# Kernel tuning notes

Hardware: AMD Instinct MI355X
Metric: run time of the kernel (lower is better)

Reference implementation:

```python
import jax, jax.numpy as jnp
import numpy as np

DK = 128
B, S = 16, 2048

def setup_inputs() -> dict:
    key = jax.random.key(0)
    kq, kk, kv = jax.random.split(key, 3)
    q = jax.random.normal(kq, (B, S, DK), dtype=jnp.float32)
    k = jax.random.normal(kk, (B, S, DK), dtype=jnp.float32)
    v = jax.random.normal(kv, (B, S, DK), dtype=jnp.float32)
    return {"q": q, "k": k, "v": v}

def reference(q, k, v):
    # scores: [B, S, S]
    scale = 1.0 / jnp.sqrt(jnp.float32(DK))
    scores = jnp.einsum("bqd,bkd->bqk", q, k) * scale
    probs = jax.nn.softmax(scores, axis=-1)
    # dropout is identity in eval mode (training=None)
    return jnp.einsum("bqk,bkd->bqd", probs, v)
```

## Files before the change

kernel.cpp:

```cpp
#include <hip/hip_runtime.h>
#include <hip/hip_bf16.h>

#define BATCH 16
#define SEQ   2048
#define DK    128
#define NT    16
#define SC2   0.12751744f
#define THRL2 11.541560f

typedef __attribute__((ext_vector_type(8)))  short short8v;
typedef __attribute__((ext_vector_type(4)))  float float4v;
typedef __attribute__((ext_vector_type(16))) float float16v;

typedef const __attribute__((address_space(1))) unsigned int* gas_t;
typedef __attribute__((address_space(3))) unsigned int* las_t;

__device__ inline void gl_lds16(const void* g, void* l) {
    __builtin_amdgcn_global_load_lds((gas_t)g, (las_t)l, 16, 0, 0);
}

__device__ inline short f2bf(float f) {
    __hip_bfloat16 h = __float2bfloat16(f);
    unsigned short u;
    __builtin_memcpy(&u, &h, sizeof(u));
    return (short)u;
}

__device__ inline unsigned cvt_pk_bf16(float a, float b) {
    unsigned r;
    asm("v_cvt_pk_bf16_f32 %0, %1, %2" : "=v"(r) : "v"(a), "v"(b));
    return r;
}

__global__ __launch_bounds__(256)
void conv_k_kernel(const float* __restrict__ k, short* __restrict__ kb)
{
    size_t i = ((size_t)blockIdx.x * 256 + threadIdx.x) * 8;
    float4 a = *reinterpret_cast<const float4*>(k + i);
    float4 b = *reinterpret_cast<const float4*>(k + i + 4);
    short8v t;
    t[0] = f2bf(a.x * SC2); t[1] = f2bf(a.y * SC2); t[2] = f2bf(a.z * SC2); t[3] = f2bf(a.w * SC2);
    t[4] = f2bf(b.x * SC2); t[5] = f2bf(b.y * SC2); t[6] = f2bf(b.z * SC2); t[7] = f2bf(b.w * SC2);
    *reinterpret_cast<short8v*>(kb + i) = t;
}

__global__ __launch_bounds__(256)
void transpose_v_kernel(const float* __restrict__ v, short* __restrict__ vt)
{
    __shared__ float tile[32][33];
    const int tx = threadIdx.x & 31;
    const int ty = threadIdx.x >> 5;
    const int b  = blockIdx.z;
    const int s0 = blockIdx.x * 32;
    const int d0 = blockIdx.y * 32;

    const float* vb = v + ((size_t)b * SEQ + s0) * DK + d0;
#pragma unroll
    for (int i = 0; i < 4; ++i) {
        int r = ty + 8 * i;
        tile[r][tx] = vb[(size_t)r * DK + tx];
    }
    __syncthreads();

    const int s   = s0 + tx;
    const int kvl = s & 15;
    const int pos = (((kvl >> 2) & 1) << 3) | (((kvl >> 3) & 1) << 2) | (kvl & 3);
    const size_t col = (size_t)(s & ~15) | pos;

    short* vtb = vt + ((size_t)b * DK + d0) * SEQ;
#pragma unroll
    for (int i = 0; i < 4; ++i) {
        int r = ty + 8 * i;
        vtb[(size_t)r * SEQ + col] = f2bf(tile[tx][r]);
    }
}

__global__ __launch_bounds__(512, 2)
void attn_fwd_v6(const float* __restrict__ q,
                 const short* __restrict__ kb,
                 const short* __restrict__ vt,
                 float* __restrict__ out)
{
    __shared__ __align__(16) char lds[131072];

    const int tid  = threadIdx.x;
    const int lane = tid & 63;
    const int wave = tid >> 6;
    const int qt   = wave & 3;
    const int h    = wave >> 2;
    const int b    = blockIdx.y;
    const int q0   = blockIdx.x * 128 + qt * 32;

    const int l31 = lane & 31;
    const int hi  = lane >> 5;

    const float* qrow = q + ((size_t)b * SEQ + q0 + l31) * DK + hi * 8;
    short8v qf[8];
#pragma unroll
    for (int s = 0; s < 8; ++s) {
        float4 x = *reinterpret_cast<const float4*>(qrow + s * 16);
        float4 y = *reinterpret_cast<const float4*>(qrow + s * 16 + 4);
        union { unsigned u[4]; short8v v; } pk;
        pk.u[0] = cvt_pk_bf16(x.x, x.y);
        pk.u[1] = cvt_pk_bf16(x.z, x.w);
        pk.u[2] = cvt_pk_bf16(y.x, y.y);
        pk.u[3] = cvt_pk_bf16(y.z, y.w);
        qf[s] = pk.v;
    }

    const char* kB = (const char*)(kb + (size_t)b * SEQ * DK);
    const char* vB = (const char*)(vt + (size_t)b * DK * SEQ);
    const int hkv = h * 1024;

    const char* src[8];
    int dstoff[8];
    long sstep;
    if (qt < 2) {
#pragma unroll
        for (int i = 0; i < 8; ++i) {
            const int kr = qt * 32 + i * 4 + (lane >> 4);
            src[i] = kB + (size_t)(hkv + kr) * 256 + (((lane & 15) ^ (kr & 15)) << 4);
            dstoff[i] = h * 32768 + qt * 8192 + i * 1024;
        }
        sstep = 64 * 256;
    } else {
#pragma unroll
        for (int i = 0; i < 8; ++i) {
            const int R  = (qt - 2) * 32 + i * 4 + (lane >> 4);
            const int wx = (lane & 15) ^ (R & 15);
            const int d  = 2 * R + (wx >> 3);
            src[i] = vB + (size_t)d * (SEQ * 2) + (size_t)hkv * 2 + ((wx & 7) << 4);
            dstoff[i] = h * 32768 + 16384 + (qt - 2) * 8192 + i * 1024;
        }
        sstep = 64 * 2;
    }

    float m_run = -1e30f;
    float l_run = 0.0f;
    float16v o[4];
#pragma unroll
    for (int dblk = 0; dblk < 4; ++dblk)
#pragma unroll
        for (int i = 0; i < 16; ++i) o[dblk][i] = 0.f;

    auto STAGE = [&](int bufsel, int t) {
        char* base = lds + bufsel * 65536;
#pragma unroll
        for (int i = 0; i < 8; ++i)
            gl_lds16(src[i] + (size_t)t * sstep, base + dstoff[i]);
    };

    STAGE(0, 0);
    __syncthreads();

    int buf = 0;
    for (int t = 0; t < NT; ++t) {
        if (t + 1 < NT) STAGE(buf ^ 1, t + 1);

        const char* Kl = lds + buf * 65536 + h * 32768;
        const char* Vl = Kl + 16384;
        const char* ka = Kl + l31 * 256;

        float16v sa[2];
#pragma unroll
        for (int i = 0; i < 16; ++i) { sa[0][i] = 0.f; sa[1][i] = 0.f; }
        __builtin_amdgcn_s_setprio(1);
#pragma unroll
        for (int s = 0; s < 8; ++s) {
            const int un = ((2 * s + hi) ^ (l31 & 15)) << 4;
            short8v kf0 = *reinterpret_cast<const short8v*>(ka + un);
            short8v kf1 = *reinterpret_cast<const short8v*>(ka + 8192 + un);
            sa[0] = __builtin_amdgcn_mfma_f32_32x32x16_bf16(kf0, qf[s], sa[0], 0, 0, 0);
            sa[1] = __builtin_amdgcn_mfma_f32_32x32x16_bf16(kf1, qf[s], sa[1], 0, 0, 0);
        }
        __builtin_amdgcn_s_setprio(0);

        float mx = sa[0][0];
#pragma unroll
        for (int i = 1; i < 16; ++i) mx = fmaxf(mx, sa[0][i]);
#pragma unroll
        for (int i = 0; i < 16; ++i) mx = fmaxf(mx, sa[1][i]);
        mx = fmaxf(mx, __shfl_xor(mx, 32));

        if (!__all(mx <= m_run + THRL2)) {
            const float mnew  = fmaxf(m_run, mx);
            const float alpha = exp2f(m_run - mnew);
            l_run *= alpha;
            m_run = mnew;
            float aq[16];
#pragma unroll
            for (int reg = 0; reg < 16; ++reg)
                aq[reg] = __shfl(alpha, (reg & 3) + 8 * (reg >> 2) + 4 * hi);
#pragma unroll
            for (int dblk = 0; dblk < 4; ++dblk)
#pragma unroll
                for (int reg = 0; reg < 16; ++reg) o[dblk][reg] *= aq[reg];
        }

        float ts = 0.f;
#pragma unroll
        for (int sub = 0; sub < 2; ++sub)
#pragma unroll
            for (int i = 0; i < 16; ++i) {
                const float e = exp2f(sa[sub][i] - m_run);
                sa[sub][i] = e;
                ts += e;
            }
        ts += __shfl_xor(ts, 32);
        l_run += ts;

        short8v pf[4];
#pragma unroll
        for (int g = 0; g < 4; ++g) {
            const int sub = g >> 1, r0 = (g & 1) * 8;
            union { unsigned u[4]; short8v v; } pk;
            pk.u[0] = cvt_pk_bf16(sa[sub][r0 + 0], sa[sub][r0 + 1]);
            pk.u[1] = cvt_pk_bf16(sa[sub][r0 + 2], sa[sub][r0 + 3]);
            pk.u[2] = cvt_pk_bf16(sa[sub][r0 + 4], sa[sub][r0 + 5]);
            pk.u[3] = cvt_pk_bf16(sa[sub][r0 + 6], sa[sub][r0 + 7]);
            pf[g] = pk.v;
        }

        __builtin_amdgcn_s_setprio(1);
#pragma unroll
        for (int dblk = 0; dblk < 4; ++dblk) {
            const int R  = dblk * 16 + (l31 >> 1);
            const char* vr = Vl + R * 256;
            const int dh = (l31 & 1) << 3;
#pragma unroll
            for (int g = 0; g < 4; ++g) {
                const int w = ((dh | (2 * g + hi)) ^ (R & 15)) << 4;
                short8v vf = *reinterpret_cast<const short8v*>(vr + w);
                o[dblk] = __builtin_amdgcn_mfma_f32_32x32x16_bf16(pf[g], vf, o[dblk], 0, 0, 0);
            }
        }
        __builtin_amdgcn_s_setprio(0);

        __syncthreads();
        buf ^= 1;
    }

    float* smO = (float*)lds;
    float* smM = (float*)(lds + 65536);
    float* smL = (float*)(lds + 66048);

    if (h == 1) {
        if (hi == 0) { smM[qt * 32 + l31] = m_run; smL[qt * 32 + l31] = l_run; }
#pragma unroll
        for (int dblk = 0; dblk < 4; ++dblk)
#pragma unroll
            for (int reg = 0; reg < 16; ++reg) {
                const int qp = (reg & 3) + 8 * (reg >> 2) + 4 * hi;
                smO[(qt * 32 + qp) * 128 + dblk * 32 + l31] = o[dblk][reg];
            }
    }
    __syncthreads();
    if (h == 0) {
        const float m1 = smM[qt * 32 + l31];
        const float l1 = smL[qt * 32 + l31];
        const float mf = fmaxf(m_run, m1);
        const float a0 = exp2f(m_run - mf);
        const float a1 = exp2f(m1 - mf);
        const float li = 1.0f / (l_run * a0 + l1 * a1);
        const float w0 = a0 * li;
        const float w1 = a1 * li;

        float w0q[16], w1q[16];
#pragma unroll
        for (int reg = 0; reg < 16; ++reg) {
            const int qp = (reg & 3) + 8 * (reg >> 2) + 4 * hi;
            w0q[reg] = __shfl(w0, qp);
            w1q[reg] = __shfl(w1, qp);
        }

        float* ob = out + ((size_t)b * SEQ + q0) * DK;
#pragma unroll
        for (int dblk = 0; dblk < 4; ++dblk)
#pragma unroll
            for (int reg = 0; reg < 16; ++reg) {
                const int qp = (reg & 3) + 8 * (reg >> 2) + 4 * hi;
                ob[(size_t)qp * DK + dblk * 32 + l31] =
                    o[dblk][reg] * w0q[reg]
                    + smO[(qt * 32 + qp) * 128 + dblk * 32 + l31] * w1q[reg];
            }
    }
}

__global__ __launch_bounds__(256)
void attn_fwd_slow(const float* __restrict__ q,
                   const float* __restrict__ k,
                   const float* __restrict__ v,
                   float* __restrict__ out)
{
    const int lane = threadIdx.x & 63;
    const int wave = threadIdx.x >> 6;
    const int b    = blockIdx.y;
    const int q0   = blockIdx.x * 64 + wave * 16;
    const int row = lane & 15;
    const int grp = lane >> 4;

    const float* qb = q + ((size_t)b * SEQ + q0) * DK;
    const float* kbp = k + (size_t)b * SEQ * DK;
    const float* vbp = v + (size_t)b * SEQ * DK;

    short8v qf[4];
#pragma unroll
    for (int c = 0; c < 4; ++c) {
        const float* p = qb + row * DK + c * 32 + grp * 8;
        float4 x = *reinterpret_cast<const float4*>(p);
        float4 y = *reinterpret_cast<const float4*>(p + 4);
        short8v t;
        t[0] = f2bf(x.x); t[1] = f2bf(x.y); t[2] = f2bf(x.z); t[3] = f2bf(x.w);
        t[4] = f2bf(y.x); t[5] = f2bf(y.y); t[6] = f2bf(y.z); t[7] = f2bf(y.w);
        qf[c] = t;
    }

    float m_run = -1e30f, l_run = 0.0f;
    float4v o[8];
#pragma unroll
    for (int i = 0; i < 8; ++i) { o[i][0]=0.f; o[i][1]=0.f; o[i][2]=0.f; o[i][3]=0.f; }
    const float scale = 0.08838834764831845f;

    for (int kv0 = 0; kv0 < SEQ; kv0 += 16) {
        short8v kf[4];
        const float* kp0 = kbp + (size_t)(kv0 + row) * DK + grp * 8;
#pragma unroll
        for (int c = 0; c < 4; ++c) {
            const float* p = kp0 + c * 32;
            float4 x = *reinterpret_cast<const float4*>(p);
            float4 y = *reinterpret_cast<const float4*>(p + 4);
            short8v t;
            t[0] = f2bf(x.x); t[1] = f2bf(x.y); t[2] = f2bf(x.z); t[3] = f2bf(x.w);
            t[4] = f2bf(y.x); t[5] = f2bf(y.y); t[6] = f2bf(y.z); t[7] = f2bf(y.w);
            kf[c] = t;
        }
        short8v vf[8];
#pragma unroll
        for (int dblk = 0; dblk < 8; ++dblk) {
            const float* p = vbp + (size_t)(kv0 + 4 * grp) * DK + dblk * 16 + row;
            short b0 = f2bf(p[0]);
            short b1 = f2bf(p[DK]);
            short b2 = f2bf(p[2 * DK]);
            short b3 = f2bf(p[3 * DK]);
            short8v t;
            t[0]=b0; t[1]=b1; t[2]=b2; t[3]=b3; t[4]=b0; t[5]=b1; t[6]=b2; t[7]=b3;
            vf[dblk] = t;
        }
        float4v s; s[0]=0.f; s[1]=0.f; s[2]=0.f; s[3]=0.f;
#pragma unroll
        for (int c = 0; c < 4; ++c)
            s = __builtin_amdgcn_mfma_f32_16x16x32_bf16(kf[c], qf[c], s, 0, 0, 0);

        float sv[4]; float tmax = -1e30f;
#pragma unroll
        for (int r = 0; r < 4; ++r) { sv[r] = s[r] * scale; tmax = fmaxf(tmax, sv[r]); }
        tmax = fmaxf(tmax, __shfl_xor(tmax, 16));
        tmax = fmaxf(tmax, __shfl_xor(tmax, 32));
        const float mnew = fmaxf(m_run, tmax);
        float pr[4]; float tsum = 0.f;
#pragma unroll
        for (int r = 0; r < 4; ++r) { pr[r] = __expf(sv[r] - mnew); tsum += pr[r]; }
        tsum += __shfl_xor(tsum, 16);
        tsum += __shfl_xor(tsum, 32);
        const float alpha = __expf(m_run - mnew);
        l_run = l_run * alpha + tsum;
        m_run = mnew;
        float aq[4];
#pragma unroll
        for (int r = 0; r < 4; ++r) aq[r] = __shfl(alpha, grp * 4 + r);
#pragma unroll
        for (int dblk = 0; dblk < 8; ++dblk)
#pragma unroll
            for (int r = 0; r < 4; ++r) o[dblk][r] *= aq[r];

        short8v pfv;
        pfv[0]=f2bf(pr[0]); pfv[1]=f2bf(pr[1]); pfv[2]=f2bf(pr[2]); pfv[3]=f2bf(pr[3]);
        pfv[4]=0; pfv[5]=0; pfv[6]=0; pfv[7]=0;
#pragma unroll
        for (int dblk = 0; dblk < 8; ++dblk)
            o[dblk] = __builtin_amdgcn_mfma_f32_16x16x32_bf16(pfv, vf[dblk], o[dblk], 0, 0, 0);
    }

    const float linv = 1.0f / l_run;
    float li[4];
#pragma unroll
    for (int r = 0; r < 4; ++r) li[r] = __shfl(linv, grp * 4 + r);
    float* ob = out + ((size_t)b * SEQ + q0) * DK;
#pragma unroll
    for (int dblk = 0; dblk < 8; ++dblk)
#pragma unroll
        for (int r = 0; r < 4; ++r)
            ob[(size_t)(grp * 4 + r) * DK + dblk * 16 + row] = o[dblk][r] * li[r];
}

extern "C" void kernel_launch(void* const* d_in, const int* in_sizes, int n_in,
                              void* d_out, int out_size, void* d_ws, size_t ws_size,
                              hipStream_t stream) {
    const float* q = (const float*)d_in[0];
    const float* k = (const float*)d_in[1];
    const float* v = (const float*)d_in[2];
    float* out = (float*)d_out;

    const size_t kb_bytes = (size_t)BATCH * SEQ * DK * sizeof(short);
    const size_t need = 2 * kb_bytes;

    if (ws_size >= need) {
        short* kb = (short*)d_ws;
        short* vt = (short*)((char*)d_ws + kb_bytes);
        hipLaunchKernelGGL(conv_k_kernel, dim3(2048), dim3(256), 0, stream, k, kb);
        hipLaunchKernelGGL(transpose_v_kernel, dim3(SEQ / 32, DK / 32, BATCH), dim3(256), 0, stream, v, vt);
        hipLaunchKernelGGL(attn_fwd_v6, dim3(SEQ / 128, BATCH), dim3(512), 0, stream, q, kb, vt, out);
    } else {
        hipLaunchKernelGGL(attn_fwd_slow, dim3(SEQ / 64, BATCH), dim3(256), 0, stream, q, k, v, out);
    }
}
```

Measured before the change: 64.62 us.

## Halve KV tile to 32 keys, shrink LDS, raise occupancy and swizzle block mapping

Each KV tile now holds 32 keys per half instead of 64, so the flash loop runs twice as many iterations with half the LDS per buffer. LDS drops to about 65KB and the launch bound asks for 4 blocks per CU instead of 2, which should help hide latency. Staging is rebalanced so waves 0-3 load K and waves 4-7 load V, with a new swizzle pattern for the V tile. The grid is flattened to 1D with an XCD-aware remap that keeps same-batch blocks together for L2 reuse. The cost is more barriers and more softmax rescale checks per key, and less MFMA work per synchronization.

```diff
diff --git a/kernel.cpp b/kernel.cpp
--- a/kernel.cpp
+++ b/kernel.cpp
@@ -4,7 +4,7 @@
 #define BATCH 16
 #define SEQ   2048
 #define DK    128
-#define NT    16
+#define NT    32
 #define SC2   0.12751744f
 #define THRL2 11.541560f
 
@@ -75,21 +75,23 @@
     }
 }
 
-__global__ __launch_bounds__(512, 2)
-void attn_fwd_v6(const float* __restrict__ q,
+__global__ __launch_bounds__(512, 4)
+void attn_fwd_v7(const float* __restrict__ q,
                  const short* __restrict__ kb,
                  const short* __restrict__ vt,
                  float* __restrict__ out)
 {
-    __shared__ __align__(16) char lds[131072];
+    __shared__ __align__(16) char lds[66560];
 
     const int tid  = threadIdx.x;
     const int lane = tid & 63;
     const int wave = tid >> 6;
     const int qt   = wave & 3;
     const int h    = wave >> 2;
-    const int b    = blockIdx.y;
-    const int q0   = blockIdx.x * 128 + qt * 32;
+    const int bid  = blockIdx.x;
+    const int work = (bid & 7) * 32 + (bid >> 3);
+    const int b    = work >> 4;
+    const int q0   = (work & 15) * 128 + qt * 32;
 
     const int l31 = lane & 31;
     const int hi  = lane >> 5;
@@ -110,29 +112,33 @@
 
     const char* kB = (const char*)(kb + (size_t)b * SEQ * DK);
     const char* vB = (const char*)(vt + (size_t)b * DK * SEQ);
-    const int hkv = h * 1024;
-
-    const char* src[8];
-    int dstoff[8];
+
+    const char* src[4];
+    int dstoff[4];
     long sstep;
-    if (qt < 2) {
-#pragma unroll
-        for (int i = 0; i < 8; ++i) {
-            const int kr = qt * 32 + i * 4 + (lane >> 4);
-            src[i] = kB + (size_t)(hkv + kr) * 256 + (((lane & 15) ^ (kr & 15)) << 4);
-            dstoff[i] = h * 32768 + qt * 8192 + i * 1024;
-        }
-        sstep = 64 * 256;
+    if (wave < 4) {
+#pragma unroll
+        for (int i = 0; i < 4; ++i) {
+            const int c  = wave * 4 + i;
+            const int hh = c >> 3, cc = c & 7;
+            const int kr = cc * 4 + (lane >> 4);
+            src[i] = kB + (size_t)(hh * 1024 + kr) * 256
+                        + (((lane & 15) ^ (kr & 15)) << 4);
+            dstoff[i] = hh * 16384 + cc * 1024;
+        }
+        sstep = 32 * 256;
     } else {
 #pragma unroll
-        for (int i = 0; i < 8; ++i) {
-            const int R  = (qt - 2) * 32 + i * 4 + (lane >> 4);
-            const int wx = (lane & 15) ^ (R & 15);
-            const int d  = 2 * R + (wx >> 3);
-            src[i] = vB + (size_t)d * (SEQ * 2) + (size_t)hkv * 2 + ((wx & 7) << 4);
-            dstoff[i] = h * 32768 + 16384 + (qt - 2) * 8192 + i * 1024;
-        }
-        sstep = 64 * 2;
+        for (int i = 0; i < 4; ++i) {
+            const int c    = (wave - 4) * 4 + i;
+            const int hh   = c >> 3, cc = c & 7;
+            const int R    = cc * 8 + (lane >> 3);
+            const int unit = (lane & 7) ^ (R & 7);
+            const int d    = 2 * R + (unit >> 2);
+            src[i] = vB + (size_t)d * (SEQ * 2) + hh * 2048 + (unit & 3) * 16;
+            dstoff[i] = hh * 16384 + 8192 + cc * 1024;
+        }
+        sstep = 32 * 2;
     }
 
     float m_run = -1e30f;
@@ -144,9 +150,9 @@
         for (int i = 0; i < 16; ++i) o[dblk][i] = 0.f;
 
     auto STAGE = [&](int bufsel, int t) {
-        char* base = lds + bufsel * 65536;
-#pragma unroll
-        for (int i = 0; i < 8; ++i)
+        char* base = lds + bufsel * 32768;
+#pragma unroll
+        for (int i = 0; i < 4; ++i)
             gl_lds16(src[i] + (size_t)t * sstep, base + dstoff[i]);
     };
 
@@ -157,29 +163,25 @@
     for (int t = 0; t < NT; ++t) {
         if (t + 1 < NT) STAGE(buf ^ 1, t + 1);
 
-        const char* Kl = lds + buf * 65536 + h * 32768;
-        const char* Vl = Kl + 16384;
+        const char* Kl = lds + buf * 32768 + h * 16384;
+        const char* Vl = Kl + 8192;
         const char* ka = Kl + l31 * 256;
 
-        float16v sa[2];
-#pragma unroll
-        for (int i = 0; i < 16; ++i) { sa[0][i] = 0.f; sa[1][i] = 0.f; }
+        float16v sa;
+#pragma unroll
+        for (int i = 0; i < 16; ++i) sa[i] = 0.f;
         __builtin_amdgcn_s_setprio(1);
 #pragma unroll
         for (int s = 0; s < 8; ++s) {
             const int un = ((2 * s + hi) ^ (l31 & 15)) << 4;
-            short8v kf0 = *reinterpret_cast<const short8v*>(ka + un);
-            short8v kf1 = *reinterpret_cast<const short8v*>(ka + 8192 + un);
-            sa[0] = __builtin_amdgcn_mfma_f32_32x32x16_bf16(kf0, qf[s], sa[0], 0, 0, 0);
-            sa[1] = __builtin_amdgcn_mfma_f32_32x32x16_bf16(kf1, qf[s], sa[1], 0, 0, 0);
+            short8v kf = *reinterpret_cast<const short8v*>(ka + un);
+            sa = __builtin_amdgcn_mfma_f32_32x32x16_bf16(kf, qf[s], sa, 0, 0, 0);
         }
         __builtin_amdgcn_s_setprio(0);
 
-        float mx = sa[0][0];
-#pragma unroll
-        for (int i = 1; i < 16; ++i) mx = fmaxf(mx, sa[0][i]);
-#pragma unroll
-        for (int i = 0; i < 16; ++i) mx = fmaxf(mx, sa[1][i]);
+        float mx = sa[0];
+#pragma unroll
+        for (int i = 1; i < 16; ++i) mx = fmaxf(mx, sa[i]);
         mx = fmaxf(mx, __shfl_xor(mx, 32));
 
         if (!__all(mx <= m_run + THRL2)) {
@@ -199,25 +201,23 @@
 
         float ts = 0.f;
 #pragma unroll
-        for (int sub = 0; sub < 2; ++sub)
-#pragma unroll
-            for (int i = 0; i < 16; ++i) {
-                const float e = exp2f(sa[sub][i] - m_run);
-                sa[sub][i] = e;
-                ts += e;
-            }
+        for (int i = 0; i < 16; ++i) {
+            const float e = exp2f(sa[i] - m_run);
+            sa[i] = e;
+            ts += e;
+        }
         ts += __shfl_xor(ts, 32);
         l_run += ts;
 
-        short8v pf[4];
-#pragma unroll
-        for (int g = 0; g < 4; ++g) {
-            const int sub = g >> 1, r0 = (g & 1) * 8;
+        short8v pf[2];
+#pragma unroll
+        for (int g = 0; g < 2; ++g) {
+            const int r0 = g * 8;
             union { unsigned u[4]; short8v v; } pk;
-            pk.u[0] = cvt_pk_bf16(sa[sub][r0 + 0], sa[sub][r0 + 1]);
-            pk.u[1] = cvt_pk_bf16(sa[sub][r0 + 2], sa[sub][r0 + 3]);
-            pk.u[2] = cvt_pk_bf16(sa[sub][r0 + 4], sa[sub][r0 + 5]);
-            pk.u[3] = cvt_pk_bf16(sa[sub][r0 + 6], sa[sub][r0 + 7]);
+            pk.u[0] = cvt_pk_bf16(sa[r0 + 0], sa[r0 + 1]);
+            pk.u[1] = cvt_pk_bf16(sa[r0 + 2], sa[r0 + 3]);
+            pk.u[2] = cvt_pk_bf16(sa[r0 + 4], sa[r0 + 5]);
+            pk.u[3] = cvt_pk_bf16(sa[r0 + 6], sa[r0 + 7]);
             pf[g] = pk.v;
         }
 
@@ -225,11 +225,11 @@
 #pragma unroll
         for (int dblk = 0; dblk < 4; ++dblk) {
             const int R  = dblk * 16 + (l31 >> 1);
-            const char* vr = Vl + R * 256;
-            const int dh = (l31 & 1) << 3;
-#pragma unroll
-            for (int g = 0; g < 4; ++g) {
-                const int w = ((dh | (2 * g + hi)) ^ (R & 15)) << 4;
+            const char* vr = Vl + R * 128;
+            const int dh4 = (l31 & 1) << 2;
+#pragma unroll
+            for (int g = 0; g < 2; ++g) {
+                const int w = ((dh4 | (2 * g + hi)) ^ (R & 7)) << 4;
                 short8v vf = *reinterpret_cast<const short8v*>(vr + w);
                 o[dblk] = __builtin_amdgcn_mfma_f32_32x32x16_bf16(pf[g], vf, o[dblk], 0, 0, 0);
             }
@@ -409,7 +409,7 @@
         short* vt = (short*)((char*)d_ws + kb_bytes);
         hipLaunchKernelGGL(conv_k_kernel, dim3(2048), dim3(256), 0, stream, k, kb);
         hipLaunchKernelGGL(transpose_v_kernel, dim3(SEQ / 32, DK / 32, BATCH), dim3(256), 0, stream, v, vt);
-        hipLaunchKernelGGL(attn_fwd_v6, dim3(SEQ / 128, BATCH), dim3(512), 0, stream, q, kb, vt, out);
+        hipLaunchKernelGGL(attn_fwd_v7, dim3((SEQ / 128) * BATCH), dim3(512), 0, stream, q, kb, vt, out);
     } else {
         hipLaunchKernelGGL(attn_fwd_slow, dim3(SEQ / 64, BATCH), dim3(256), 0, stream, q, k, v, out);
     }
```

Result: slower. 156.8 us (+142.7%).
